# Kernel optimization log

Measured on AMD Instinct MI355X. Metric: run time of the kernel, lower is better.

The kernel has to match this reference:

```python
import jax, jax.numpy as jnp
import numpy as np

N = 16384
E = 65536

def _nnconv(x, src, dst, edge_attr, A, b, root, bias, c_in, c_out):
    # edge MLP: [E,2] -> [E, c_in*c_out], ReLU
    W = jax.nn.relu(edge_attr @ A + b).reshape(E, c_in, c_out)
    # gather source features, per-edge matmul: [E,c_in] x [E,c_in,c_out] -> [E,c_out]
    msg = jnp.einsum('ei,eio->eo', x[src], W)
    # scatter-add to target nodes
    agg = jax.ops.segment_sum(msg, dst, num_segments=N)
    return agg + x @ root + bias

def setup_inputs() -> dict:
    key = jax.random.key(0)
    ks = jax.random.split(key, 12)
    inp = {
        'x': jax.random.normal(ks[0], (N, 8), dtype=jnp.float32),
        'edge_index': jax.random.randint(ks[1], (2, E), 0, N, dtype=jnp.int64),
        'edge_attr': jax.random.normal(ks[2], (E, 2), dtype=jnp.float32),
        # edge-MLP 1: Linear(2, 512)
        'A1': jax.random.normal(ks[3], (2, 512), dtype=jnp.float32) * (1.0 / np.sqrt(2.0)),
        'b1': jnp.zeros((512,), dtype=jnp.float32),
        # edge-MLP 2: Linear(2, 4096)
        'A2': jax.random.normal(ks[4], (2, 4096), dtype=jnp.float32) * (1.0 / np.sqrt(2.0)),
        'b2': jnp.zeros((4096,), dtype=jnp.float32),
        # NNConv root weights + biases
        'root1': jax.random.normal(ks[5], (8, 64), dtype=jnp.float32) * (1.0 / np.sqrt(8.0)),
        'bias1': jnp.zeros((64,), dtype=jnp.float32),
        'root2': jax.random.normal(ks[6], (64, 64), dtype=jnp.float32) * (1.0 / np.sqrt(64.0)),
        'bias2': jnp.zeros((64,), dtype=jnp.float32),
    }
    return inp

def reference(x, edge_index, edge_attr, A1, b1, A2, b2, root1, bias1, root2, bias2):
    src = edge_index[0]  # x_j (message source)
    dst = edge_index[1]  # aggregation target
    h = _nnconv(x, src, dst, edge_attr, A1, b1, root1, bias1, 8, 64)
    h = _nnconv(h, src, dst, edge_attr, A2, b2, root2, bias2, 64, 64)
    return h
```

## Files before the change

kernel.cpp:

```cpp
#include <hip/hip_runtime.h>

#define N_NODES 16384
#define N_EDGES 65536

typedef float f32x16 __attribute__((ext_vector_type(16)));
typedef float f32x8  __attribute__((ext_vector_type(8)));

__device__ __forceinline__ float rfl_f(float v) {
    int i = __builtin_amdgcn_readfirstlane(__builtin_bit_cast(int, v));
    return __builtin_bit_cast(float, i);
}

__global__ void k_node1(const float* __restrict__ x, const float* __restrict__ root1,
                        const float* __restrict__ bias1, float* __restrict__ h1) {
    int t = blockIdx.x * blockDim.x + threadIdx.x;
    int n = t >> 6, o = t & 63;
    float acc = bias1[o];
#pragma unroll
    for (int i = 0; i < 8; ++i)
        acc = fmaf(x[n * 8 + i], root1[i * 64 + o], acc);
    h1[t] = acc;
}

__global__ __launch_bounds__(256)
void k_edge1(const float* __restrict__ x, const int* __restrict__ ei,
             const float* __restrict__ ea, const float* __restrict__ A1,
             const float* __restrict__ b1, float* __restrict__ h1) {
    int lane = threadIdx.x & 63;
    f32x8 W0, W1, BB;
#pragma unroll
    for (int i = 0; i < 8; ++i) {
        W0[i] = A1[i * 64 + lane];
        W1[i] = A1[512 + i * 64 + lane];
        BB[i] = b1[i * 64 + lane];
    }
    asm volatile("" : "+v"(W0), "+v"(W1), "+v"(BB));

    int wid = blockIdx.x * (blockDim.x >> 6) + (threadIdx.x >> 6);
    int nw = gridDim.x * (blockDim.x >> 6);
#pragma clang loop unroll(disable)
    for (int p = wid; p < N_EDGES / 2; p += nw) {
        int2 srcp = ((const int2*)ei)[p];
        int2 dstp = ((const int2*)(ei + N_EDGES))[p];
        float4 eap = ((const float4*)ea)[p];
        int s0 = __builtin_amdgcn_readfirstlane(srcp.x);
        int s1 = __builtin_amdgcn_readfirstlane(srcp.y);
        int d0 = __builtin_amdgcn_readfirstlane(dstp.x);
        int d1 = __builtin_amdgcn_readfirstlane(dstp.y);
        float ea00 = rfl_f(eap.x), ea01 = rfl_f(eap.y);
        float ea10 = rfl_f(eap.z), ea11 = rfl_f(eap.w);
        const float* xp0 = x + (size_t)s0 * 8;
        const float* xp1 = x + (size_t)s1 * 8;
        f32x8 ha, hb;
        asm volatile("s_load_dwordx8 %0, %2, 0x0\n\t"
                     "s_load_dwordx8 %1, %3, 0x0\n\t"
                     "s_waitcnt lgkmcnt(0)"
                     : "=s"(ha), "=s"(hb) : "s"(xp0), "s"(xp1));
        float acc0 = 0.f, acc1 = 0.f;
#pragma unroll
        for (int i = 0; i < 8; ++i) {
            float wva = fmaxf(fmaf(ea01, W1[i], fmaf(ea00, W0[i], BB[i])), 0.f);
            acc0 = fmaf(ha[i], wva, acc0);
            float wvb = fmaxf(fmaf(ea11, W1[i], fmaf(ea10, W0[i], BB[i])), 0.f);
            acc1 = fmaf(hb[i], wvb, acc1);
        }
        atomicAdd(&h1[(size_t)d0 * 64 + lane], acc0);
        atomicAdd(&h1[(size_t)d1 * 64 + lane], acc1);
    }
}

__global__ __launch_bounds__(256) __attribute__((amdgpu_waves_per_eu(4, 4)))
void k_node2(const float* __restrict__ h1, const float* __restrict__ root2,
             const float* __restrict__ bias2, float* __restrict__ out) {
    int lane = threadIdx.x & 63;
    f32x16 R0, R1, R2, R3;
#pragma unroll
    for (int i = 0; i < 16; ++i) {
        R0[i] = root2[(i)      * 64 + lane];
        R1[i] = root2[(16 + i) * 64 + lane];
        R2[i] = root2[(32 + i) * 64 + lane];
        R3[i] = root2[(48 + i) * 64 + lane];
    }
    asm volatile("" : "+v"(R0), "+v"(R1), "+v"(R2), "+v"(R3));
    float bias = bias2[lane];

    int wid = blockIdx.x * (blockDim.x >> 6) + (threadIdx.x >> 6);
    int nw = gridDim.x * (blockDim.x >> 6);
#pragma clang loop unroll(disable)
    for (int n = wid; n < N_NODES; n += nw) {
        int nu = __builtin_amdgcn_readfirstlane(n);
        const float* hp = h1 + (size_t)nu * 64;
        f32x16 h0, h1v, h2, h3;
        asm volatile("s_load_dwordx16 %0, %4, 0x0\n\t"
                     "s_load_dwordx16 %1, %4, 0x40\n\t"
                     "s_load_dwordx16 %2, %4, 0x80\n\t"
                     "s_load_dwordx16 %3, %4, 0xc0\n\t"
                     "s_waitcnt lgkmcnt(0)"
                     : "=s"(h0), "=s"(h1v), "=s"(h2), "=s"(h3) : "s"(hp));
        float acc = bias;
#pragma unroll
        for (int i = 0; i < 16; ++i) acc = fmaf(h0[i],  R0[i], acc);
#pragma unroll
        for (int i = 0; i < 16; ++i) acc = fmaf(h1v[i], R1[i], acc);
#pragma unroll
        for (int i = 0; i < 16; ++i) acc = fmaf(h2[i],  R2[i], acc);
#pragma unroll
        for (int i = 0; i < 16; ++i) acc = fmaf(h3[i],  R3[i], acc);
        out[(size_t)nu * 64 + lane] = acc;
    }
}

__global__ __launch_bounds__(256) __attribute__((amdgpu_waves_per_eu(2, 2)))
void k_edge2(const float* __restrict__ h1, const int* __restrict__ ei,
             const float* __restrict__ ea, const float* __restrict__ A2,
             const float* __restrict__ b2, float* __restrict__ out) {
    int lane = threadIdx.x & 63;
    int wid = blockIdx.x * (blockDim.x >> 6) + (threadIdx.x >> 6);
    int nw = gridDim.x * (blockDim.x >> 6);
    int base = __builtin_amdgcn_readfirstlane((wid & 1) * 32);

    f32x16 W0a, W0b, W1a, W1b, Ba, Bb;
#pragma unroll
    for (int i = 0; i < 16; ++i) {
        W0a[i] = A2[(base + i)      * 64 + lane];
        W0b[i] = A2[(base + 16 + i) * 64 + lane];
        W1a[i] = A2[4096 + (base + i)      * 64 + lane];
        W1b[i] = A2[4096 + (base + 16 + i) * 64 + lane];
        Ba[i]  = b2[(base + i)      * 64 + lane];
        Bb[i]  = b2[(base + 16 + i) * 64 + lane];
    }
    asm volatile("" : "+v"(W0a), "+v"(W0b), "+v"(W1a), "+v"(W1b), "+v"(Ba), "+v"(Bb));

#pragma clang loop unroll(disable)
    for (int p = wid >> 1; p < N_EDGES / 2; p += (nw >> 1)) {
        int2 srcp = ((const int2*)ei)[p];
        int2 dstp = ((const int2*)(ei + N_EDGES))[p];
        float4 eap = ((const float4*)ea)[p];
        int s0 = __builtin_amdgcn_readfirstlane(srcp.x);
        int s1 = __builtin_amdgcn_readfirstlane(srcp.y);
        int d0 = __builtin_amdgcn_readfirstlane(dstp.x);
        int d1 = __builtin_amdgcn_readfirstlane(dstp.y);
        float ea00 = rfl_f(eap.x), ea01 = rfl_f(eap.y);
        float ea10 = rfl_f(eap.z), ea11 = rfl_f(eap.w);
        const float* hp0 = h1 + (size_t)s0 * 64 + base;
        const float* hp1 = h1 + (size_t)s1 * 64 + base;
        f32x16 ha, hb, hc, hd;
        asm volatile("s_load_dwordx16 %0, %4, 0x0\n\t"
                     "s_load_dwordx16 %1, %4, 0x40\n\t"
                     "s_load_dwordx16 %2, %5, 0x0\n\t"
                     "s_load_dwordx16 %3, %5, 0x40\n\t"
                     "s_waitcnt lgkmcnt(0)"
                     : "=s"(ha), "=s"(hb), "=s"(hc), "=s"(hd)
                     : "s"(hp0), "s"(hp1));
        float acc0 = 0.f, acc1 = 0.f;
#pragma unroll
        for (int i = 0; i < 16; ++i) {
            float wva = fmaxf(fmaf(ea01, W1a[i], fmaf(ea00, W0a[i], Ba[i])), 0.f);
            acc0 = fmaf(ha[i], wva, acc0);
            float wvb = fmaxf(fmaf(ea11, W1a[i], fmaf(ea10, W0a[i], Ba[i])), 0.f);
            acc1 = fmaf(hc[i], wvb, acc1);
        }
#pragma unroll
        for (int i = 0; i < 16; ++i) {
            float wva = fmaxf(fmaf(ea01, W1b[i], fmaf(ea00, W0b[i], Bb[i])), 0.f);
            acc0 = fmaf(hb[i], wva, acc0);
            float wvb = fmaxf(fmaf(ea11, W1b[i], fmaf(ea10, W0b[i], Bb[i])), 0.f);
            acc1 = fmaf(hd[i], wvb, acc1);
        }
        atomicAdd(&out[(size_t)d0 * 64 + lane], acc0);
        atomicAdd(&out[(size_t)d1 * 64 + lane], acc1);
    }
}

extern "C" void kernel_launch(void* const* d_in, const int* in_sizes, int n_in,
                              void* d_out, int out_size, void* d_ws, size_t ws_size,
                              hipStream_t stream) {
    const float* x     = (const float*)d_in[0];
    const int*   ei    = (const int*)d_in[1];
    const float* ea    = (const float*)d_in[2];
    const float* A1    = (const float*)d_in[3];
    const float* b1    = (const float*)d_in[4];
    const float* A2    = (const float*)d_in[5];
    const float* b2    = (const float*)d_in[6];
    const float* root1 = (const float*)d_in[7];
    const float* bias1 = (const float*)d_in[8];
    const float* root2 = (const float*)d_in[9];
    const float* bias2 = (const float*)d_in[10];
    float* out = (float*)d_out;
    float* h1  = (float*)d_ws;

    k_node1<<<N_NODES * 64 / 256, 256, 0, stream>>>(x, root1, bias1, h1);
    k_edge1<<<2048, 256, 0, stream>>>(x, ei, ea, A1, b1, h1);
    k_node2<<<1024, 256, 0, stream>>>(h1, root2, bias2, out);
    k_edge2<<<2048, 256, 0, stream>>>(h1, ei, ea, A2, b2, out);
}
```

Measured before the change: 155.6 us.

## Stage edge2 MLP weights in LDS instead of registers and raise occupancy

```diff
diff --git a/kernel.cpp b/kernel.cpp
--- a/kernel.cpp
+++ b/kernel.cpp
@@ -5,6 +5,7 @@
 
 typedef float f32x16 __attribute__((ext_vector_type(16)));
 typedef float f32x8  __attribute__((ext_vector_type(8)));
+typedef float f32x4  __attribute__((ext_vector_type(4)));
 
 __device__ __forceinline__ float rfl_f(float v) {
     int i = __builtin_amdgcn_readfirstlane(__builtin_bit_cast(int, v));
@@ -55,7 +56,7 @@
         asm volatile("s_load_dwordx8 %0, %2, 0x0\n\t"
                      "s_load_dwordx8 %1, %3, 0x0\n\t"
                      "s_waitcnt lgkmcnt(0)"
-                     : "=s"(ha), "=s"(hb) : "s"(xp0), "s"(xp1));
+                     : "=&s"(ha), "=&s"(hb) : "s"(xp0), "s"(xp1));
         float acc0 = 0.f, acc1 = 0.f;
 #pragma unroll
         for (int i = 0; i < 8; ++i) {
@@ -69,7 +70,7 @@
     }
 }
 
-__global__ __launch_bounds__(256) __attribute__((amdgpu_waves_per_eu(4, 4)))
+__global__ __launch_bounds__(256)
 void k_node2(const float* __restrict__ h1, const float* __restrict__ root2,
              const float* __restrict__ bias2, float* __restrict__ out) {
     int lane = threadIdx.x & 63;
@@ -96,7 +97,7 @@
                      "s_load_dwordx16 %2, %4, 0x80\n\t"
                      "s_load_dwordx16 %3, %4, 0xc0\n\t"
                      "s_waitcnt lgkmcnt(0)"
-                     : "=s"(h0), "=s"(h1v), "=s"(h2), "=s"(h3) : "s"(hp));
+                     : "=&s"(h0), "=&s"(h1v), "=&s"(h2), "=&s"(h3) : "s"(hp));
         float acc = bias;
 #pragma unroll
         for (int i = 0; i < 16; ++i) acc = fmaf(h0[i],  R0[i], acc);
@@ -110,29 +111,28 @@
     }
 }
 
-__global__ __launch_bounds__(256) __attribute__((amdgpu_waves_per_eu(2, 2)))
+__global__ __launch_bounds__(256)
 void k_edge2(const float* __restrict__ h1, const int* __restrict__ ei,
              const float* __restrict__ ea, const float* __restrict__ A2,
              const float* __restrict__ b2, float* __restrict__ out) {
+    __shared__ __align__(16) float WT[3 * 64 * 36];
+    int half = blockIdx.x & 1;
+    for (int j = threadIdx.x; j < 2048; j += 256) {
+        int i = j >> 6, o = j & 63;
+        WT[o * 36 + i]                = A2[half * 2048 + j];
+        WT[64 * 36 + o * 36 + i]      = A2[4096 + half * 2048 + j];
+        WT[2 * 64 * 36 + o * 36 + i]  = b2[half * 2048 + j];
+    }
+    __syncthreads();
+
     int lane = threadIdx.x & 63;
-    int wid = blockIdx.x * (blockDim.x >> 6) + (threadIdx.x >> 6);
-    int nw = gridDim.x * (blockDim.x >> 6);
-    int base = __builtin_amdgcn_readfirstlane((wid & 1) * 32);
-
-    f32x16 W0a, W0b, W1a, W1b, Ba, Bb;
-#pragma unroll
-    for (int i = 0; i < 16; ++i) {
-        W0a[i] = A2[(base + i)      * 64 + lane];
-        W0b[i] = A2[(base + 16 + i) * 64 + lane];
-        W1a[i] = A2[4096 + (base + i)      * 64 + lane];
-        W1b[i] = A2[4096 + (base + 16 + i) * 64 + lane];
-        Ba[i]  = b2[(base + i)      * 64 + lane];
-        Bb[i]  = b2[(base + 16 + i) * 64 + lane];
-    }
-    asm volatile("" : "+v"(W0a), "+v"(W0b), "+v"(W1a), "+v"(W1b), "+v"(Ba), "+v"(Bb));
-
+    int base = half * 32;
+    unsigned laddr = (unsigned)(uintptr_t)WT + lane * 144;
+
+    int g = blockIdx.x >> 1;
+    int wslot = g * 4 + (threadIdx.x >> 6);
 #pragma clang loop unroll(disable)
-    for (int p = wid >> 1; p < N_EDGES / 2; p += (nw >> 1)) {
+    for (int p = wslot; p < N_EDGES / 2; p += 4096) {
         int2 srcp = ((const int2*)ei)[p];
         int2 dstp = ((const int2*)(ei + N_EDGES))[p];
         float4 eap = ((const float4*)ea)[p];
@@ -144,28 +144,79 @@
         float ea10 = rfl_f(eap.z), ea11 = rfl_f(eap.w);
         const float* hp0 = h1 + (size_t)s0 * 64 + base;
         const float* hp1 = h1 + (size_t)s1 * 64 + base;
+
         f32x16 ha, hb, hc, hd;
         asm volatile("s_load_dwordx16 %0, %4, 0x0\n\t"
                      "s_load_dwordx16 %1, %4, 0x40\n\t"
                      "s_load_dwordx16 %2, %5, 0x0\n\t"
-                     "s_load_dwordx16 %3, %5, 0x40\n\t"
-                     "s_waitcnt lgkmcnt(0)"
-                     : "=s"(ha), "=s"(hb), "=s"(hc), "=s"(hd)
+                     "s_load_dwordx16 %3, %5, 0x40"
+                     : "=&s"(ha), "=&s"(hb), "=&s"(hc), "=&s"(hd)
                      : "s"(hp0), "s"(hp1));
+
+        f32x4 wa[8], wb[8], wc[8];
+        asm volatile(
+            "ds_read_b128 %0, %12 offset:0\n\t"
+            "ds_read_b128 %1, %12 offset:16\n\t"
+            "ds_read_b128 %2, %12 offset:32\n\t"
+            "ds_read_b128 %3, %12 offset:48\n\t"
+            "ds_read_b128 %4, %12 offset:9216\n\t"
+            "ds_read_b128 %5, %12 offset:9232\n\t"
+            "ds_read_b128 %6, %12 offset:9248\n\t"
+            "ds_read_b128 %7, %12 offset:9264\n\t"
+            "ds_read_b128 %8, %12 offset:18432\n\t"
+            "ds_read_b128 %9, %12 offset:18448\n\t"
+            "ds_read_b128 %10, %12 offset:18464\n\t"
+            "ds_read_b128 %11, %12 offset:18480"
+            : "=&v"(wa[0]), "=&v"(wa[1]), "=&v"(wa[2]), "=&v"(wa[3]),
+              "=&v"(wb[0]), "=&v"(wb[1]), "=&v"(wb[2]), "=&v"(wb[3]),
+              "=&v"(wc[0]), "=&v"(wc[1]), "=&v"(wc[2]), "=&v"(wc[3])
+            : "v"(laddr));
+        asm volatile(
+            "ds_read_b128 %0, %12 offset:64\n\t"
+            "ds_read_b128 %1, %12 offset:80\n\t"
+            "ds_read_b128 %2, %12 offset:96\n\t"
+            "ds_read_b128 %3, %12 offset:112\n\t"
+            "ds_read_b128 %4, %12 offset:9280\n\t"
+            "ds_read_b128 %5, %12 offset:9296\n\t"
+            "ds_read_b128 %6, %12 offset:9312\n\t"
+            "ds_read_b128 %7, %12 offset:9328\n\t"
+            "ds_read_b128 %8, %12 offset:18496\n\t"
+            "ds_read_b128 %9, %12 offset:18512\n\t"
+            "ds_read_b128 %10, %12 offset:18528\n\t"
+            "ds_read_b128 %11, %12 offset:18544"
+            : "=&v"(wa[4]), "=&v"(wa[5]), "=&v"(wa[6]), "=&v"(wa[7]),
+              "=&v"(wb[4]), "=&v"(wb[5]), "=&v"(wb[6]), "=&v"(wb[7]),
+              "=&v"(wc[4]), "=&v"(wc[5]), "=&v"(wc[6]), "=&v"(wc[7])
+            : "v"(laddr));
+        asm volatile("s_waitcnt lgkmcnt(0)"
+            : "+v"(wa[0]), "+v"(wa[1]), "+v"(wa[2]), "+v"(wa[3]),
+              "+v"(wa[4]), "+v"(wa[5]), "+v"(wa[6]), "+v"(wa[7]),
+              "+v"(wb[0]), "+v"(wb[1]), "+v"(wb[2]), "+v"(wb[3]),
+              "+v"(wb[4]), "+v"(wb[5]), "+v"(wb[6]), "+v"(wb[7]),
+              "+v"(wc[0]), "+v"(wc[1]), "+v"(wc[2]), "+v"(wc[3]),
+              "+v"(wc[4]), "+v"(wc[5]), "+v"(wc[6]), "+v"(wc[7]),
+              "+s"(ha), "+s"(hb), "+s"(hc), "+s"(hd));
+
         float acc0 = 0.f, acc1 = 0.f;
 #pragma unroll
-        for (int i = 0; i < 16; ++i) {
-            float wva = fmaxf(fmaf(ea01, W1a[i], fmaf(ea00, W0a[i], Ba[i])), 0.f);
-            acc0 = fmaf(ha[i], wva, acc0);
-            float wvb = fmaxf(fmaf(ea11, W1a[i], fmaf(ea10, W0a[i], Ba[i])), 0.f);
-            acc1 = fmaf(hc[i], wvb, acc1);
+        for (int q = 0; q < 4; ++q) {
+#pragma unroll
+            for (int k = 0; k < 4; ++k) {
+                float wv0 = fmaxf(fmaf(ea01, wb[q][k], fmaf(ea00, wa[q][k], wc[q][k])), 0.f);
+                acc0 = fmaf(ha[q * 4 + k], wv0, acc0);
+                float wv1 = fmaxf(fmaf(ea11, wb[q][k], fmaf(ea10, wa[q][k], wc[q][k])), 0.f);
+                acc1 = fmaf(hc[q * 4 + k], wv1, acc1);
+            }
         }
 #pragma unroll
-        for (int i = 0; i < 16; ++i) {
-            float wva = fmaxf(fmaf(ea01, W1b[i], fmaf(ea00, W0b[i], Bb[i])), 0.f);
-            acc0 = fmaf(hb[i], wva, acc0);
-            float wvb = fmaxf(fmaf(ea11, W1b[i], fmaf(ea10, W0b[i], Bb[i])), 0.f);
-            acc1 = fmaf(hd[i], wvb, acc1);
+        for (int q = 4; q < 8; ++q) {
+#pragma unroll
+            for (int k = 0; k < 4; ++k) {
+                float wv0 = fmaxf(fmaf(ea01, wb[q][k], fmaf(ea00, wa[q][k], wc[q][k])), 0.f);
+                acc0 = fmaf(hb[(q - 4) * 4 + k], wv0, acc0);
+                float wv1 = fmaxf(fmaf(ea11, wb[q][k], fmaf(ea10, wa[q][k], wc[q][k])), 0.f);
+                acc1 = fmaf(hd[(q - 4) * 4 + k], wv1, acc1);
+            }
         }
         atomicAdd(&out[(size_t)d0 * 64 + lane], acc0);
         atomicAdd(&out[(size_t)d1 * 64 + lane], acc1);
```

Measured after the change: 144.3 us. -7.3%, faster.
